# Kernel optimization log

Measured on AMD Instinct MI355X. Metric: run time of the kernel, lower is better.

The kernel has to match this reference:

```python
import jax, jax.numpy as jnp
import numpy as np

D_MODEL = 768
NUM_HEADS = 12
D_K = D_MODEL // NUM_HEADS


def setup_inputs() -> dict:
    key = jax.random.key(0)
    ks = jax.random.split(key, 5)
    B, S = 2, 2048
    scale = 1.0 / np.sqrt(D_MODEL)
    return {
        "x": jax.random.normal(ks[0], (B, S, D_MODEL), dtype=jnp.float32),
        "q_proj_weight": jax.random.normal(ks[1], (D_MODEL, D_MODEL), dtype=jnp.float32) * scale,
        "k_proj_weight": jax.random.normal(ks[2], (D_MODEL, D_MODEL), dtype=jnp.float32) * scale,
        "v_proj_weight": jax.random.normal(ks[3], (D_MODEL, D_MODEL), dtype=jnp.float32) * scale,
        "o_proj_weight": jax.random.normal(ks[4], (D_MODEL, D_MODEL), dtype=jnp.float32) * scale,
    }


def reference(x, q_proj_weight, k_proj_weight, v_proj_weight, o_proj_weight):
    B, S, _ = x.shape
    H, dk = NUM_HEADS, D_K
    # projections: weight is [d_out, d_in], applied as x @ W^T
    Q = jnp.einsum("bsd,ed->bse", x, q_proj_weight).reshape(B, S, H, dk)
    K = jnp.einsum("bsd,ed->bse", x, k_proj_weight).reshape(B, S, H, dk)
    V = jnp.einsum("bsd,ed->bse", x, v_proj_weight).reshape(B, S, H, dk)
    # scores [b, h, q, k]
    scores = jnp.einsum("bqhd,bkhd->bhqk", Q, K) / jnp.sqrt(jnp.float32(dk))
    causal = jnp.tril(jnp.ones((S, S), dtype=bool))
    scores = jnp.where(causal, scores, -jnp.inf)
    attn = jax.nn.softmax(scores, axis=-1)
    out = jnp.einsum("bhqk,bkhd->bqhd", attn, V).reshape(B, S, H * dk)
    return jnp.einsum("bsd,ed->bse", out, o_proj_weight)
```

## Files before the change

kernel.cpp:

```cpp
#include <hip/hip_runtime.h>
#include <hip/hip_bf16.h>
#include <stdint.h>

typedef __hip_bfloat16 bf16;
typedef __attribute__((ext_vector_type(8))) short short8;
typedef __attribute__((ext_vector_type(4))) float f32x4;
typedef __attribute__((ext_vector_type(16))) float f32x16;

#define MFMA16(A, B, C) __builtin_amdgcn_mfma_f32_16x16x32_bf16(A, B, C, 0, 0, 0)
#define MFMA32(A, B, C) __builtin_amdgcn_mfma_f32_32x32x16_bf16(A, B, C, 0, 0, 0)

#define SB 2
#define SS 2048
#define SD 768
#define SH 12
#define SM (SB*SS)
#define BHSD (SB*SH*SS*64)
#define QSCALE 0.18033688011112042f

__device__ __forceinline__ void gload_lds16(const bf16* g, bf16* l) {
    __builtin_amdgcn_global_load_lds(
        (const __attribute__((address_space(1))) void*)(g),
        (__attribute__((address_space(3))) void*)(l),
        16, 0, 0);
}

__device__ __forceinline__ int cvtpk(float a, float b) {
    int r;
    asm("v_cvt_pk_bf16_f32 %0, %1, %2" : "=v"(r) : "v"(a), "v"(b));
    return r;
}
__device__ __forceinline__ void plswap(int& a, int& b) {
    asm("v_permlane32_swap_b32 %0, %1" : "+v"(a), "+v"(b));
}

__global__ void cvt_all(const float4* __restrict__ x,  const float4* __restrict__ w0,
                        const float4* __restrict__ w1, const float4* __restrict__ w2,
                        const float4* __restrict__ w3,
                        uint64_t* __restrict__ xb, uint64_t* __restrict__ wqkv,
                        uint64_t* __restrict__ wob) {
    int bid = blockIdx.x;
    const float4* s; uint64_t* d; int base;
    if (bid < 3072) { s = x; d = xb; base = bid << 8; }
    else {
        int t = bid - 3072, seg = t / 576, li = t - seg * 576;
        s = (seg == 0) ? w0 : (seg == 1) ? w1 : (seg == 2) ? w2 : w3;
        d = (seg < 3) ? (wqkv + seg * 147456) : wob;
        base = li << 8;
    }
    int i = base + threadIdx.x;
    float4 v = s[i];
    union { bf16 h[4]; uint64_t u; } p;
    p.h[0] = __float2bfloat16(v.x);
    p.h[1] = __float2bfloat16(v.y);
    p.h[2] = __float2bfloat16(v.z);
    p.h[3] = __float2bfloat16(v.w);
    d[i] = p.u;
}

template<int EPI>
__global__ __launch_bounds__(256) void gemm_bt(const bf16* __restrict__ A,
                                               const bf16* __restrict__ Bw,
                                               void* __restrict__ Out,
                                               int K) {
    __shared__ bf16 lA[128 * 64];
    __shared__ bf16 lB[128 * 64];
    const int tid  = threadIdx.x;
    const int lane = tid & 63;
    const int wid  = tid >> 6;
    const int wr = wid >> 1, wc = wid & 1;
    const int m0 = blockIdx.y * 128, n0 = blockIdx.x * 128;
    const int g = lane >> 4, l15 = lane & 15;
    const int srow = lane >> 3, slot = lane & 7;

    f32x4 acc[4][4] = {};

    for (int kt = 0; kt < K; kt += 64) {
        __syncthreads();
        #pragma unroll
        for (int p = 0; p < 4; ++p) {
            int c = wid * 4 + p;
            int row = c * 8 + srow;
            int colsw = (slot ^ (row & 7)) * 8;
            gload_lds16(A  + (m0 + row) * K + kt + colsw, &lA[c * 512]);
            gload_lds16(Bw + (n0 + row) * K + kt + colsw, &lB[c * 512]);
        }
        __syncthreads();
        #pragma unroll
        for (int ks = 0; ks < 2; ++ks) {
            short8 af[4], bfv[4];
            #pragma unroll
            for (int m = 0; m < 4; ++m) {
                int row = wr * 64 + m * 16 + l15;
                int idx = row * 64 + (((ks * 4 + g) ^ (row & 7)) * 8);
                af[m] = *reinterpret_cast<const short8*>(&lA[idx]);
            }
            #pragma unroll
            for (int n = 0; n < 4; ++n) {
                int row = wc * 64 + n * 16 + l15;
                int idx = row * 64 + (((ks * 4 + g) ^ (row & 7)) * 8);
                bfv[n] = *reinterpret_cast<const short8*>(&lB[idx]);
            }
            #pragma unroll
            for (int m = 0; m < 4; ++m)
                #pragma unroll
                for (int n = 0; n < 4; ++n)
                    acc[m][n] = MFMA16(af[m], bfv[n], acc[m][n]);
        }
    }

    #pragma unroll
    for (int m = 0; m < 4; ++m) {
        #pragma unroll
        for (int n = 0; n < 4; ++n) {
            int col = n0 + wc * 64 + n * 16 + l15;
            #pragma unroll
            for (int r = 0; r < 4; ++r) {
                int row = m0 + wr * 64 + m * 16 + g * 4 + r;
                float v = acc[m][n][r];
                if constexpr (EPI == 0) {
                    int which = (col >= 1536) ? 2 : (col >= 768 ? 1 : 0);
                    int e = col - which * 768;
                    int h = e >> 6, d = e & 63;
                    int b = row >> 11, s = row & 2047;
                    int bh = b * SH + h;
                    bf16* dst = (bf16*)Out;
                    int idx;
                    if (which == 2) idx = 2 * BHSD + (bh * 64 + d) * SS + s;
                    else            idx = which * BHSD + (bh * SS + s) * 64 + d;
                    if (which == 0) v *= QSCALE;
                    dst[idx] = __float2bfloat16(v);
                } else {
                    ((float*)Out)[row * SD + col] = v;
                }
            }
        }
    }
}

__global__ __launch_bounds__(64) void attn_kernel(const bf16* __restrict__ Qb,
                                                  const bf16* __restrict__ Kb,
                                                  const bf16* __restrict__ Vtb,
                                                  bf16* __restrict__ AO) {
    __shared__ float bc[32];

    const int orig = blockIdx.x;
    const int xcd = orig & 7, li = orig >> 3;
    const int bh = xcd * 3 + (li >> 6);
    const int p = li & 63;
    const int j = (p < 32) ? (63 - p) : (p - 32);

    const int b = bh / SH, h = bh - b * SH;
    const int lane = threadIdx.x;
    const int l31 = lane & 31, hi = lane >> 5;

    const bf16* Qh = Qb + bh * SS * 64;
    const bf16* Kh = Kb + bh * SS * 64;
    const bf16* Vh = Vtb + bh * 64 * SS;

    const int qself = j * 32 + l31;
    short8 qf[4];
    #pragma unroll
    for (int ks = 0; ks < 4; ++ks)
        qf[ks] = *reinterpret_cast<const short8*>(Qh + qself * 64 + ks * 16 + hi * 8);

    f32x16 oacc[2];
    #pragma unroll
    for (int n = 0; n < 2; ++n)
        #pragma unroll
        for (int r = 0; r < 16; ++r) oacc[n][r] = 0.f;
    float mrow = -1e30f, lrow = 0.f;

    const bf16* kbase = Kh + l31 * 64 + hi * 8;
    const bf16* vbase = Vh + l31 * SS + hi * 8;

#define LDG(pp) (*reinterpret_cast<const short8*>(pp))

#define LOADSET(K0, K1, K2, K3, V00, V01, V10, V11, T) do {                  \
    const bf16* kp_ = kbase + (T) * 2048;                                    \
    K0 = LDG(kp_); K1 = LDG(kp_ + 16); K2 = LDG(kp_ + 32); K3 = LDG(kp_ + 48); \
    const bf16* vp_ = vbase + (T) * 32;                                      \
    V00 = LDG(vp_); V01 = LDG(vp_ + 16);                                     \
    V10 = LDG(vp_ + 65536); V11 = LDG(vp_ + 65536 + 16);                     \
} while (0)

#define TILE_BODY(K0, K1, K2, K3, V00, V01, V10, V11, KT) do {               \
    f32x16 sacc;                                                             \
    _Pragma("unroll")                                                        \
    for (int r = 0; r < 16; ++r) sacc[r] = 0.f;                              \
    __builtin_amdgcn_s_setprio(1);                                           \
    sacc = MFMA32(K0, qf[0], sacc);                                          \
    sacc = MFMA32(K1, qf[1], sacc);                                          \
    sacc = MFMA32(K2, qf[2], sacc);                                          \
    sacc = MFMA32(K3, qf[3], sacc);                                          \
    __builtin_amdgcn_s_setprio(0);                                           \
    if ((KT) == j) {                                                         \
        _Pragma("unroll")                                                    \
        for (int r = 0; r < 16; ++r) {                                       \
            int kvrow = (r & 3) + 8 * (r >> 2) + 4 * hi;                     \
            if (kvrow > l31) sacc[r] = -1e30f;                               \
        }                                                                    \
    }                                                                        \
    float t0 = fmaxf(fmaxf(sacc[0],  sacc[1]),  fmaxf(sacc[2],  sacc[3]));   \
    float t1 = fmaxf(fmaxf(sacc[4],  sacc[5]),  fmaxf(sacc[6],  sacc[7]));   \
    float t2 = fmaxf(fmaxf(sacc[8],  sacc[9]),  fmaxf(sacc[10], sacc[11]));  \
    float t3 = fmaxf(fmaxf(sacc[12], sacc[13]), fmaxf(sacc[14], sacc[15]));  \
    float pm = fmaxf(fmaxf(t0, t1), fmaxf(t2, t3));                          \
    pm = fmaxf(pm, __shfl_xor(pm, 32));                                      \
    if (__any(pm > mrow + 8.f)) {                                            \
        float mn = fmaxf(mrow, pm);                                          \
        float sf = exp2f(mrow - mn);                                         \
        mrow = mn;                                                           \
        lrow *= sf;                                                          \
        if (lane < 32) bc[lane] = sf;                                        \
        f32x4 sv0 = *reinterpret_cast<f32x4*>(&bc[ 0 + 4 * hi]);             \
        f32x4 sv1 = *reinterpret_cast<f32x4*>(&bc[ 8 + 4 * hi]);             \
        f32x4 sv2 = *reinterpret_cast<f32x4*>(&bc[16 + 4 * hi]);             \
        f32x4 sv3 = *reinterpret_cast<f32x4*>(&bc[24 + 4 * hi]);             \
        _Pragma("unroll")                                                    \
        for (int n = 0; n < 2; ++n) {                                        \
            _Pragma("unroll")                                                \
            for (int r = 0; r < 16; ++r) {                                   \
                float f_ = (r >> 2) == 0 ? sv0[r & 3] :                      \
                           (r >> 2) == 1 ? sv1[r & 3] :                      \
                           (r >> 2) == 2 ? sv2[r & 3] : sv3[r & 3];          \
                oacc[n][r] *= f_;                                            \
            }                                                                \
        }                                                                    \
    }                                                                        \
    _Pragma("unroll")                                                        \
    for (int r = 0; r < 16; ++r) sacc[r] = exp2f(sacc[r] - mrow);            \
    float s0 = (sacc[0] + sacc[1]) + (sacc[2] + sacc[3]);                    \
    float s1 = (sacc[4] + sacc[5]) + (sacc[6] + sacc[7]);                    \
    float s2 = (sacc[8] + sacc[9]) + (sacc[10] + sacc[11]);                  \
    float s3 = (sacc[12] + sacc[13]) + (sacc[14] + sacc[15]);                \
    float rs = (s0 + s1) + (s2 + s3);                                        \
    rs += __shfl_xor(rs, 32);                                                \
    lrow += rs;                                                              \
    int a0 = cvtpk(sacc[0],  sacc[1]),  a1 = cvtpk(sacc[2],  sacc[3]);       \
    int b0 = cvtpk(sacc[4],  sacc[5]),  b1 = cvtpk(sacc[6],  sacc[7]);       \
    plswap(a0, b0); plswap(a1, b1);                                          \
    int a2 = cvtpk(sacc[8],  sacc[9]),  a3 = cvtpk(sacc[10], sacc[11]);      \
    int b2 = cvtpk(sacc[12], sacc[13]), b3 = cvtpk(sacc[14], sacc[15]);      \
    plswap(a2, b2); plswap(a3, b3);                                          \
    union { int wd[4]; short8 s8; } u0_, u1_;                                \
    u0_.wd[0] = a0; u0_.wd[1] = a1; u0_.wd[2] = b0; u0_.wd[3] = b1;          \
    u1_.wd[0] = a2; u1_.wd[1] = a3; u1_.wd[2] = b2; u1_.wd[3] = b3;          \
    __builtin_amdgcn_s_setprio(1);                                           \
    oacc[0] = MFMA32(u0_.s8, V00, oacc[0]);                                  \
    oacc[0] = MFMA32(u1_.s8, V01, oacc[0]);                                  \
    oacc[1] = MFMA32(u0_.s8, V10, oacc[1]);                                  \
    oacc[1] = MFMA32(u1_.s8, V11, oacc[1]);                                  \
    __builtin_amdgcn_s_setprio(0);                                           \
} while (0)

    short8 ka0, ka1, ka2, ka3, va00, va01, va10, va11;
    short8 kb0, kb1, kb2, kb3, vb00, vb01, vb10, vb11;

    LOADSET(ka0, ka1, ka2, ka3, va00, va01, va10, va11, 0);
    LOADSET(kb0, kb1, kb2, kb3, vb00, vb01, vb10, vb11, 1);

    int kt = 0;
    for (;;) {
        TILE_BODY(ka0, ka1, ka2, ka3, va00, va01, va10, va11, kt);
        LOADSET(ka0, ka1, ka2, ka3, va00, va01, va10, va11, kt + 2);
        ++kt;
        if (kt > j) break;
        TILE_BODY(kb0, kb1, kb2, kb3, vb00, vb01, vb10, vb11, kt);
        LOADSET(kb0, kb1, kb2, kb3, vb00, vb01, vb10, vb11, kt + 2);
        ++kt;
        if (kt > j) break;
    }

    if (lane < 32) bc[lane] = 1.0f / lrow;
    f32x4 sv0 = *reinterpret_cast<f32x4*>(&bc[ 0 + 4 * hi]);
    f32x4 sv1 = *reinterpret_cast<f32x4*>(&bc[ 8 + 4 * hi]);
    f32x4 sv2 = *reinterpret_cast<f32x4*>(&bc[16 + 4 * hi]);
    f32x4 sv3 = *reinterpret_cast<f32x4*>(&bc[24 + 4 * hi]);
    #pragma unroll
    for (int n = 0; n < 2; ++n) {
        #pragma unroll
        for (int r = 0; r < 16; ++r) {
            int q = (r & 3) + 8 * (r >> 2) + 4 * hi;
            float f_ = (r >> 2) == 0 ? sv0[r & 3] :
                       (r >> 2) == 1 ? sv1[r & 3] :
                       (r >> 2) == 2 ? sv2[r & 3] : sv3[r & 3];
            float v = oacc[n][r] * f_;
            AO[(b * SS + j * 32 + q) * SD + h * 64 + n * 32 + l31] = __float2bfloat16(v);
        }
    }
}

extern "C" void kernel_launch(void* const* d_in, const int* in_sizes, int n_in,
                              void* d_out, int out_size, void* d_ws, size_t ws_size,
                              hipStream_t stream) {
    const float* x  = (const float*)d_in[0];
    const float* wq = (const float*)d_in[1];
    const float* wk = (const float*)d_in[2];
    const float* wv = (const float*)d_in[3];
    const float* wo = (const float*)d_in[4];
    float* out = (float*)d_out;

    bf16* xb   = (bf16*)d_ws;
    bf16* wqkv = xb + SM * SD;
    bf16* wob  = wqkv + 3 * SD * SD;
    bf16* qkv  = wob + SD * SD;
    bf16* ao   = qkv + 3 * BHSD;

    cvt_all<<<3072 + 4 * 576, 256, 0, stream>>>(
        (const float4*)x, (const float4*)wq, (const float4*)wk,
        (const float4*)wv, (const float4*)wo,
        (uint64_t*)xb, (uint64_t*)wqkv, (uint64_t*)wob);

    gemm_bt<0><<<dim3(2304 / 128, SM / 128), 256, 0, stream>>>(xb, wqkv, (void*)qkv, SD);
    attn_kernel<<<1536, 64, 0, stream>>>(qkv, qkv + BHSD, qkv + 2 * BHSD, ao);
    gemm_bt<1><<<dim3(SD / 128, SM / 128), 256, 0, stream>>>(ao, wob, (void*)out, SD);
}
```

Measured before the change: 132.0 us.

## Process two 32-key KV tiles per attention iteration to halve softmax overhead

The flash-attention loop now handles a 64-key block (two 32-key tiles) per iteration. It computes two score tiles with interleaved MFMAs, does one shared row-max, rescale check and row-sum reduction, then runs eight PV MFMAs. The goal is to amortize the per-tile cross-lane reductions and rescale branch, and to expose more independent MFMA work. The cost is a doubled register set for prefetched K/V, which may reduce occupancy. Padded tiles beyond the diagonal are masked, which wastes some compute on odd diagonal blocks.

```diff
diff --git a/kernel.cpp b/kernel.cpp
--- a/kernel.cpp
+++ b/kernel.cpp
@@ -176,36 +176,59 @@
 
 #define LDG(pp) (*reinterpret_cast<const short8*>(pp))
 
-#define LOADSET(K0, K1, K2, K3, V00, V01, V10, V11, T) do {                  \
-    const bf16* kp_ = kbase + (T) * 2048;                                    \
-    K0 = LDG(kp_); K1 = LDG(kp_ + 16); K2 = LDG(kp_ + 32); K3 = LDG(kp_ + 48); \
-    const bf16* vp_ = vbase + (T) * 32;                                      \
-    V00 = LDG(vp_); V01 = LDG(vp_ + 16);                                     \
-    V10 = LDG(vp_ + 65536); V11 = LDG(vp_ + 65536 + 16);                     \
+#define LOADSET2(K00, K01, K02, K03, K10, K11, K12, K13,                     \
+                 V00, V01, V02, V03, V10, V11, V12, V13, P) do {             \
+    const bf16* kp0_ = kbase + (2 * (P)) * 2048;                             \
+    K00 = LDG(kp0_);        K01 = LDG(kp0_ + 16);                            \
+    K02 = LDG(kp0_ + 32);   K03 = LDG(kp0_ + 48);                            \
+    K10 = LDG(kp0_ + 2048); K11 = LDG(kp0_ + 2064);                          \
+    K12 = LDG(kp0_ + 2080); K13 = LDG(kp0_ + 2096);                          \
+    const bf16* vp0_ = vbase + (2 * (P)) * 32;                               \
+    V00 = LDG(vp0_);             V01 = LDG(vp0_ + 16);                       \
+    V02 = LDG(vp0_ + 65536);     V03 = LDG(vp0_ + 65536 + 16);               \
+    V10 = LDG(vp0_ + 32);        V11 = LDG(vp0_ + 48);                       \
+    V12 = LDG(vp0_ + 65536 + 32);V13 = LDG(vp0_ + 65536 + 48);               \
 } while (0)
 
-#define TILE_BODY(K0, K1, K2, K3, V00, V01, V10, V11, KT) do {               \
-    f32x16 sacc;                                                             \
+#define TILE2_BODY(K00, K01, K02, K03, K10, K11, K12, K13,                   \
+                   V00, V01, V02, V03, V10, V11, V12, V13, PT) do {          \
+    const int T0_ = 2 * (PT), T1_ = T0_ + 1;                                 \
+    f32x16 s0_, s1_;                                                         \
     _Pragma("unroll")                                                        \
-    for (int r = 0; r < 16; ++r) sacc[r] = 0.f;                              \
+    for (int r = 0; r < 16; ++r) { s0_[r] = 0.f; s1_[r] = 0.f; }             \
     __builtin_amdgcn_s_setprio(1);                                           \
-    sacc = MFMA32(K0, qf[0], sacc);                                          \
-    sacc = MFMA32(K1, qf[1], sacc);                                          \
-    sacc = MFMA32(K2, qf[2], sacc);                                          \
-    sacc = MFMA32(K3, qf[3], sacc);                                          \
+    s0_ = MFMA32(K00, qf[0], s0_);  s1_ = MFMA32(K10, qf[0], s1_);           \
+    s0_ = MFMA32(K01, qf[1], s0_);  s1_ = MFMA32(K11, qf[1], s1_);           \
+    s0_ = MFMA32(K02, qf[2], s0_);  s1_ = MFMA32(K12, qf[2], s1_);           \
+    s0_ = MFMA32(K03, qf[3], s0_);  s1_ = MFMA32(K13, qf[3], s1_);           \
     __builtin_amdgcn_s_setprio(0);                                           \
-    if ((KT) == j) {                                                         \
+    if (T0_ == j) {                                                          \
         _Pragma("unroll")                                                    \
         for (int r = 0; r < 16; ++r) {                                       \
             int kvrow = (r & 3) + 8 * (r >> 2) + 4 * hi;                     \
-            if (kvrow > l31) sacc[r] = -1e30f;                               \
+            if (kvrow > l31) s0_[r] = -1e30f;                                \
         }                                                                    \
     }                                                                        \
-    float t0 = fmaxf(fmaxf(sacc[0],  sacc[1]),  fmaxf(sacc[2],  sacc[3]));   \
-    float t1 = fmaxf(fmaxf(sacc[4],  sacc[5]),  fmaxf(sacc[6],  sacc[7]));   \
-    float t2 = fmaxf(fmaxf(sacc[8],  sacc[9]),  fmaxf(sacc[10], sacc[11]));  \
-    float t3 = fmaxf(fmaxf(sacc[12], sacc[13]), fmaxf(sacc[14], sacc[15]));  \
-    float pm = fmaxf(fmaxf(t0, t1), fmaxf(t2, t3));                          \
+    if (T1_ == j) {                                                          \
+        _Pragma("unroll")                                                    \
+        for (int r = 0; r < 16; ++r) {                                       \
+            int kvrow = (r & 3) + 8 * (r >> 2) + 4 * hi;                     \
+            if (kvrow > l31) s1_[r] = -1e30f;                                \
+        }                                                                    \
+    } else if (T1_ > j) {                                                    \
+        _Pragma("unroll")                                                    \
+        for (int r = 0; r < 16; ++r) s1_[r] = -1e30f;                        \
+    }                                                                        \
+    float t0 = fmaxf(fmaxf(s0_[0],  s0_[1]),  fmaxf(s0_[2],  s0_[3]));       \
+    float t1 = fmaxf(fmaxf(s0_[4],  s0_[5]),  fmaxf(s0_[6],  s0_[7]));       \
+    float t2 = fmaxf(fmaxf(s0_[8],  s0_[9]),  fmaxf(s0_[10], s0_[11]));      \
+    float t3 = fmaxf(fmaxf(s0_[12], s0_[13]), fmaxf(s0_[14], s0_[15]));      \
+    float t4 = fmaxf(fmaxf(s1_[0],  s1_[1]),  fmaxf(s1_[2],  s1_[3]));       \
+    float t5 = fmaxf(fmaxf(s1_[4],  s1_[5]),  fmaxf(s1_[6],  s1_[7]));       \
+    float t6 = fmaxf(fmaxf(s1_[8],  s1_[9]),  fmaxf(s1_[10], s1_[11]));      \
+    float t7 = fmaxf(fmaxf(s1_[12], s1_[13]), fmaxf(s1_[14], s1_[15]));      \
+    float pm = fmaxf(fmaxf(fmaxf(t0, t1), fmaxf(t2, t3)),                    \
+                     fmaxf(fmaxf(t4, t5), fmaxf(t6, t7)));                   \
     pm = fmaxf(pm, __shfl_xor(pm, 32));                                      \
     if (__any(pm > mrow + 8.f)) {                                            \
         float mn = fmaxf(mrow, pm);                                          \
@@ -229,47 +252,76 @@
         }                                                                    \
     }                                                                        \
     _Pragma("unroll")                                                        \
-    for (int r = 0; r < 16; ++r) sacc[r] = exp2f(sacc[r] - mrow);            \
-    float s0 = (sacc[0] + sacc[1]) + (sacc[2] + sacc[3]);                    \
-    float s1 = (sacc[4] + sacc[5]) + (sacc[6] + sacc[7]);                    \
-    float s2 = (sacc[8] + sacc[9]) + (sacc[10] + sacc[11]);                  \
-    float s3 = (sacc[12] + sacc[13]) + (sacc[14] + sacc[15]);                \
-    float rs = (s0 + s1) + (s2 + s3);                                        \
+    for (int r = 0; r < 16; ++r) {                                           \
+        s0_[r] = exp2f(s0_[r] - mrow);                                       \
+        s1_[r] = exp2f(s1_[r] - mrow);                                       \
+    }                                                                        \
+    float w0 = ((s0_[0] + s0_[1]) + (s0_[2] + s0_[3]))                       \
+             + ((s0_[4] + s0_[5]) + (s0_[6] + s0_[7]));                      \
+    float w1 = ((s0_[8] + s0_[9]) + (s0_[10] + s0_[11]))                     \
+             + ((s0_[12] + s0_[13]) + (s0_[14] + s0_[15]));                  \
+    float w2 = ((s1_[0] + s1_[1]) + (s1_[2] + s1_[3]))                       \
+             + ((s1_[4] + s1_[5]) + (s1_[6] + s1_[7]));                      \
+    float w3 = ((s1_[8] + s1_[9]) + (s1_[10] + s1_[11]))                     \
+             + ((s1_[12] + s1_[13]) + (s1_[14] + s1_[15]));                  \
+    float rs = (w0 + w1) + (w2 + w3);                                        \
     rs += __shfl_xor(rs, 32);                                                \
     lrow += rs;                                                              \
-    int a0 = cvtpk(sacc[0],  sacc[1]),  a1 = cvtpk(sacc[2],  sacc[3]);       \
-    int b0 = cvtpk(sacc[4],  sacc[5]),  b1 = cvtpk(sacc[6],  sacc[7]);       \
+    int a0 = cvtpk(s0_[0],  s0_[1]),  a1 = cvtpk(s0_[2],  s0_[3]);           \
+    int b0 = cvtpk(s0_[4],  s0_[5]),  b1 = cvtpk(s0_[6],  s0_[7]);           \
     plswap(a0, b0); plswap(a1, b1);                                          \
-    int a2 = cvtpk(sacc[8],  sacc[9]),  a3 = cvtpk(sacc[10], sacc[11]);      \
-    int b2 = cvtpk(sacc[12], sacc[13]), b3 = cvtpk(sacc[14], sacc[15]);      \
+    int a2 = cvtpk(s0_[8],  s0_[9]),  a3 = cvtpk(s0_[10], s0_[11]);          \
+    int b2 = cvtpk(s0_[12], s0_[13]), b3 = cvtpk(s0_[14], s0_[15]);          \
     plswap(a2, b2); plswap(a3, b3);                                          \
-    union { int wd[4]; short8 s8; } u0_, u1_;                                \
+    int c0 = cvtpk(s1_[0],  s1_[1]),  c1 = cvtpk(s1_[2],  s1_[3]);           \
+    int d0 = cvtpk(s1_[4],  s1_[5]),  d1 = cvtpk(s1_[6],  s1_[7]);           \
+    plswap(c0, d0); plswap(c1, d1);                                          \
+    int c2 = cvtpk(s1_[8],  s1_[9]),  c3 = cvtpk(s1_[10], s1_[11]);          \
+    int d2 = cvtpk(s1_[12], s1_[13]), d3 = cvtpk(s1_[14], s1_[15]);          \
+    plswap(c2, d2); plswap(c3, d3);                                          \
+    union { int wd[4]; short8 s8; } u0_, u1_, u2_, u3_;                      \
     u0_.wd[0] = a0; u0_.wd[1] = a1; u0_.wd[2] = b0; u0_.wd[3] = b1;          \
     u1_.wd[0] = a2; u1_.wd[1] = a3; u1_.wd[2] = b2; u1_.wd[3] = b3;          \
+    u2_.wd[0] = c0; u2_.wd[1] = c1; u2_.wd[2] = d0; u2_.wd[3] = d1;          \
+    u3_.wd[0] = c2; u3_.wd[1] = c3; u3_.wd[2] = d2; u3_.wd[3] = d3;          \
     __builtin_amdgcn_s_setprio(1);                                           \
     oacc[0] = MFMA32(u0_.s8, V00, oacc[0]);                                  \
+    oacc[1] = MFMA32(u0_.s8, V02, oacc[1]);                                  \
     oacc[0] = MFMA32(u1_.s8, V01, oacc[0]);                                  \
-    oacc[1] = MFMA32(u0_.s8, V10, oacc[1]);                                  \
-    oacc[1] = MFMA32(u1_.s8, V11, oacc[1]);                                  \
+    oacc[1] = MFMA32(u1_.s8, V03, oacc[1]);                                  \
+    oacc[0] = MFMA32(u2_.s8, V10, oacc[0]);                                  \
+    oacc[1] = MFMA32(u2_.s8, V12, oacc[1]);                                  \
+    oacc[0] = MFMA32(u3_.s8, V11, oacc[0]);                                  \
+    oacc[1] = MFMA32(u3_.s8, V13, oacc[1]);                                  \
     __builtin_amdgcn_s_setprio(0);                                           \
 } while (0)
 
-    short8 ka0, ka1, ka2, ka3, va00, va01, va10, va11;
-    short8 kb0, kb1, kb2, kb3, vb00, vb01, vb10, vb11;
-
-    LOADSET(ka0, ka1, ka2, ka3, va00, va01, va10, va11, 0);
-    LOADSET(kb0, kb1, kb2, kb3, vb00, vb01, vb10, vb11, 1);
-
-    int kt = 0;
+    short8 kA00, kA01, kA02, kA03, kA10, kA11, kA12, kA13;
+    short8 vA00, vA01, vA02, vA03, vA10, vA11, vA12, vA13;
+    short8 kB00, kB01, kB02, kB03, kB10, kB11, kB12, kB13;
+    short8 vB00, vB01, vB02, vB03, vB10, vB11, vB12, vB13;
+
+    const int jp = j >> 1;
+
+    LOADSET2(kA00,kA01,kA02,kA03,kA10,kA11,kA12,kA13,
+             vA00,vA01,vA02,vA03,vA10,vA11,vA12,vA13, 0);
+    LOADSET2(kB00,kB01,kB02,kB03,kB10,kB11,kB12,kB13,
+             vB00,vB01,vB02,vB03,vB10,vB11,vB12,vB13, 1);
+
+    int pt = 0;
     for (;;) {
-        TILE_BODY(ka0, ka1, ka2, ka3, va00, va01, va10, va11, kt);
-        LOADSET(ka0, ka1, ka2, ka3, va00, va01, va10, va11, kt + 2);
-        ++kt;
-        if (kt > j) break;
-        TILE_BODY(kb0, kb1, kb2, kb3, vb00, vb01, vb10, vb11, kt);
-        LOADSET(kb0, kb1, kb2, kb3, vb00, vb01, vb10, vb11, kt + 2);
-        ++kt;
-        if (kt > j) break;
+        TILE2_BODY(kA00,kA01,kA02,kA03,kA10,kA11,kA12,kA13,
+                   vA00,vA01,vA02,vA03,vA10,vA11,vA12,vA13, pt);
+        LOADSET2(kA00,kA01,kA02,kA03,kA10,kA11,kA12,kA13,
+                 vA00,vA01,vA02,vA03,vA10,vA11,vA12,vA13, pt + 2);
+        ++pt;
+        if (pt > jp) break;
+        TILE2_BODY(kB00,kB01,kB02,kB03,kB10,kB11,kB12,kB13,
+                   vB00,vB01,vB02,vB03,vB10,vB11,vB12,vB13, pt);
+        LOADSET2(kB00,kB01,kB02,kB03,kB10,kB11,kB12,kB13,
+                 vB00,vB01,vB02,vB03,vB10,vB11,vB12,vB13, pt + 2);
+        ++pt;
+        if (pt > jp) break;
     }
 
     if (lane < 32) bc[lane] = 1.0f / lrow;
```

New measurement: 127.9 us. -3.1%, faster.
